# Optimization experiments

Measured on AMD Instinct MI355X. Metric: run time of the kernel, lower is better.

Reference implementation:

```python
import jax, jax.numpy as jnp
import numpy as np

DIM = 1024
NUM_HEADS = 16
HEAD_DIM = DIM // NUM_HEADS
SCALE = HEAD_DIM ** -0.5


def setup_inputs() -> dict:
    key = jax.random.key(0)
    k1, k2, k3, k4 = jax.random.split(key, 4)
    B, N = 2, 2048
    x = jax.random.normal(k1, (B, N, DIM), dtype=jnp.float32)
    # qkv: Linear(dim, 3*dim, bias=False); torch stores weight as [out, in]
    W_qkv = jax.random.normal(k2, (3 * DIM, DIM), dtype=jnp.float32) * (DIM ** -0.5)
    # proj: Linear(dim, dim, bias=True)
    W_proj = jax.random.normal(k3, (DIM, DIM), dtype=jnp.float32) * (DIM ** -0.5)
    b_proj = jax.random.normal(k4, (DIM,), dtype=jnp.float32) * 0.01
    return {"x": x, "W_qkv": W_qkv, "W_proj": W_proj, "b_proj": b_proj}


def reference(x, W_qkv, W_proj, b_proj):
    B, N, C = x.shape
    H, D = NUM_HEADS, HEAD_DIM
    # qkv projection: [B,N,3C] -> [3,B,H,N,D]
    qkv = jnp.einsum('bnc,oc->bno', x, W_qkv)
    qkv = qkv.reshape(B, N, 3, H, D).transpose(2, 0, 3, 1, 4)
    q, k, v = qkv[0] * SCALE, qkv[1], qkv[2]
    # full attention matrix [B,H,N,N] (faithful to manual impl)
    attn = jnp.einsum('bhqd,bhkd->bhqk', q, k)
    attn = jax.nn.softmax(attn, axis=-1)
    # dropout p=0.0 -> identity (eval semantics)
    out = jnp.einsum('bhqk,bhkd->bhqd', attn, v)  # [B,H,N,D]
    out = out.transpose(0, 2, 1, 3).reshape(B, N, C)
    out = jnp.einsum('bnc,oc->bno', out, W_proj) + b_proj
    return out
```

## Files before the change

kernel.cpp:

```cpp
#include <hip/hip_runtime.h>
#include <math.h>

#define BATCH 2
#define NTOK  2048
#define DIMC  1024
#define NH    16
#define HD    64
#define SOFT_K2 0.18033688011112042f

typedef __bf16 bf16;
typedef __attribute__((ext_vector_type(8))) __bf16 bf16x8;
typedef __attribute__((ext_vector_type(4))) __bf16 bf16x4;
typedef __attribute__((ext_vector_type(4))) float f32x4;

__device__ __forceinline__ void load_lds16(const void* g, void* l) {
    __builtin_amdgcn_global_load_lds(
        (const __attribute__((address_space(1))) void*)g,
        (__attribute__((address_space(3))) void*)l, 16, 0, 0);
}
__device__ __forceinline__ f32x4 mfma16(bf16x8 a, bf16x8 b, f32x4 c) {
    return __builtin_amdgcn_mfma_f32_16x16x32_bf16(a, b, c, 0, 0, 0);
}

__global__ __launch_bounds__(256) void cast3(
    const float* __restrict__ x,  const float* __restrict__ w1, const float* __restrict__ w2,
    bf16* __restrict__ xb, bf16* __restrict__ w1b, bf16* __restrict__ w2b)
{
    int blk = blockIdx.x;
    const float* src; bf16* dst; size_t base;
    if (blk < 4096)      { src = x;  dst = xb;  base = (size_t)blk * 1024; }
    else if (blk < 7168) { src = w1; dst = w1b; base = (size_t)(blk - 4096) * 1024; }
    else                 { src = w2; dst = w2b; base = (size_t)(blk - 7168) * 1024; }
    size_t i = base + (size_t)threadIdx.x * 4;
    float4 v = *(const float4*)(src + i);
    bf16x4 r;
    r[0] = (bf16)v.x; r[1] = (bf16)v.y; r[2] = (bf16)v.z; r[3] = (bf16)v.w;
    *(bf16x4*)(dst + i) = r;
}


__global__ __launch_bounds__(256, 3) void gemm_qkv(
    const bf16* __restrict__ A, const bf16* __restrict__ B,
    bf16* __restrict__ Cq, bf16* __restrict__ vt,
    int M, int N, int K)
{
    __shared__ __align__(16) bf16 smem[17408];

    const int tid  = threadIdx.x;
    const int w    = tid >> 6, lane = tid & 63;
    const int wm   = w & 1,  wn = w >> 1;
    const int m0   = blockIdx.y * 128, n0 = blockIdx.x * 128;
    const int lm   = lane & 15, quad = lane >> 4;

    const bf16* Arow = A + (size_t)(m0 + (tid & 127)) * K + (tid >> 7) * 8;
    const bf16* Brow = B + (size_t)(n0 + (tid & 127)) * K + (tid >> 7) * 8;

    bf16x8 ar[4], br[4];
#define QKV_LOADREG(kt) do {                                    \
    for (int t = 0; t < 4; ++t) {                               \
        ar[t] = *(const bf16x8*)(Arow + (kt) + t * 16);         \
        br[t] = *(const bf16x8*)(Brow + (kt) + t * 16);         \
    } } while (0)
#define QKV_DSWRITE() do {                                      \
    for (int t = 0; t < 4; ++t) {                               \
        *(bf16x8*)(smem + (t * 256 + tid) * 8) = ar[t];         \
        *(bf16x8*)(smem + 8192 + (t * 256 + tid) * 8) = br[t];  \
    } } while (0)

    f32x4 acc[4][4];
    f32x4 z4 = {0.f, 0.f, 0.f, 0.f};
#pragma unroll
    for (int i = 0; i < 4; ++i)
#pragma unroll
        for (int j = 0; j < 4; ++j) acc[i][j] = z4;

    const int NI = K / 64;
    QKV_LOADREG(0);
    QKV_DSWRITE();
    __syncthreads();
    for (int it = 0; it < NI; ++it) {
        if (it + 1 < NI) QKV_LOADREG((it + 1) * 64);
#pragma unroll
        for (int s = 0; s < 2; ++s) {
            bf16x8 af[4], bf_[4];
#pragma unroll
            for (int mi = 0; mi < 4; ++mi)
                af[mi] = *(const bf16x8*)(smem
                    + ((s * 4 + quad) * 128 + wm * 64 + mi * 16 + lm) * 8);
#pragma unroll
            for (int ni = 0; ni < 4; ++ni)
                bf_[ni] = *(const bf16x8*)(smem + 8192
                    + ((s * 4 + quad) * 128 + wn * 64 + ni * 16 + lm) * 8);
#pragma unroll
            for (int mi = 0; mi < 4; ++mi)
#pragma unroll
                for (int ni = 0; ni < 4; ++ni)
                    acc[mi][ni] = mfma16(af[mi], bf_[ni], acc[mi][ni]);
        }
        __syncthreads();
        if (it + 1 < NI) QKV_DSWRITE();
        __syncthreads();
    }
#undef QKV_LOADREG
#undef QKV_DSWRITE

    if (n0 >= 2048) {
        bf16* T = smem;
#pragma unroll
        for (int ni = 0; ni < 4; ++ni) {
            const int dl = wn * 64 + ni * 16 + lm;
#pragma unroll
            for (int mi = 0; mi < 4; ++mi)
#pragma unroll
                for (int r = 0; r < 4; ++r)
                    T[dl * 136 + wm * 64 + mi * 16 + quad * 4 + r] = (bf16)acc[mi][ni][r];
        }
        __syncthreads();
        const int gcol0 = n0 - 2048;
        const int bb = m0 >> 11, tokbase = m0 & 2047;
#pragma unroll
        for (int rep = 0; rep < 8; ++rep) {
            const int g = rep * 256 + tid;
            const int d = g >> 4, tc = g & 15;
            bf16x8 v = *(const bf16x8*)&T[d * 136 + tc * 8];
            const int gcol = gcol0 + d, hh = gcol >> 6, dd = gcol & 63;
            *(bf16x8*)(vt + ((size_t)((bb * NH + hh) * HD + dd)) * NTOK + tokbase + tc * 8) = v;
        }
    } else {
#pragma unroll
        for (int ni = 0; ni < 4; ++ni) {
            const int col = n0 + wn * 64 + ni * 16 + lm;
#pragma unroll
            for (int mi = 0; mi < 4; ++mi)
#pragma unroll
                for (int r = 0; r < 4; ++r) {
                    const int row = m0 + wm * 64 + mi * 16 + quad * 4 + r;
                    Cq[(size_t)row * N + col] = (bf16)acc[mi][ni][r];
                }
        }
    }
}

__global__ __launch_bounds__(256, 3) void gemm_proj(
    const bf16* __restrict__ A, const bf16* __restrict__ B,
    const float* __restrict__ bias, float* __restrict__ C,
    int M, int N, int K)
{
    __shared__ __align__(16) bf16 smem[12288];

    const int tid  = threadIdx.x;
    const int w    = tid >> 6, lane = tid & 63;
    const int wm   = w & 1,  wn = w >> 1;
    const int m0   = blockIdx.y * 64, n0 = blockIdx.x * 128;
    const int lm   = lane & 15, quad = lane >> 4;

    const bf16* Arow = A + (size_t)(m0 + (tid & 63)) * K + (tid >> 6) * 8;
    const bf16* Brow = B + (size_t)(n0 + (tid & 127)) * K + (tid >> 7) * 8;

    bf16x8 ar[2], br[4];
#define PROJ_LOADREG(kt) do {                                   \
    for (int t = 0; t < 2; ++t)                                 \
        ar[t] = *(const bf16x8*)(Arow + (kt) + t * 32);         \
    for (int t = 0; t < 4; ++t)                                 \
        br[t] = *(const bf16x8*)(Brow + (kt) + t * 16);         \
    } while (0)
#define PROJ_DSWRITE() do {                                     \
    for (int t = 0; t < 2; ++t)                                 \
        *(bf16x8*)(smem + (t * 256 + tid) * 8) = ar[t];         \
    for (int t = 0; t < 4; ++t)                                 \
        *(bf16x8*)(smem + 4096 + (t * 256 + tid) * 8) = br[t];  \
    } while (0)

    f32x4 acc[2][4];
    f32x4 z4 = {0.f, 0.f, 0.f, 0.f};
#pragma unroll
    for (int i = 0; i < 2; ++i)
#pragma unroll
        for (int j = 0; j < 4; ++j) acc[i][j] = z4;

    const int NI = K / 64;
    PROJ_LOADREG(0);
    PROJ_DSWRITE();
    __syncthreads();
    for (int it = 0; it < NI; ++it) {
        if (it + 1 < NI) PROJ_LOADREG((it + 1) * 64);
#pragma unroll
        for (int s = 0; s < 2; ++s) {
            bf16x8 af[2], bf_[4];
#pragma unroll
            for (int mi = 0; mi < 2; ++mi)
                af[mi] = *(const bf16x8*)(smem
                    + ((s * 4 + quad) * 64 + wm * 32 + mi * 16 + lm) * 8);
#pragma unroll
            for (int ni = 0; ni < 4; ++ni)
                bf_[ni] = *(const bf16x8*)(smem + 4096
                    + ((s * 4 + quad) * 128 + wn * 64 + ni * 16 + lm) * 8);
#pragma unroll
            for (int mi = 0; mi < 2; ++mi)
#pragma unroll
                for (int ni = 0; ni < 4; ++ni)
                    acc[mi][ni] = mfma16(af[mi], bf_[ni], acc[mi][ni]);
        }
        __syncthreads();
        if (it + 1 < NI) PROJ_DSWRITE();
        __syncthreads();
    }
#undef PROJ_LOADREG
#undef PROJ_DSWRITE

#pragma unroll
    for (int ni = 0; ni < 4; ++ni) {
        const int col = n0 + wn * 64 + ni * 16 + lm;
        const float bi = bias[col];
#pragma unroll
        for (int mi = 0; mi < 2; ++mi)
#pragma unroll
            for (int r = 0; r < 4; ++r) {
                const int row = m0 + wm * 32 + mi * 16 + quad * 4 + r;
                C[(size_t)row * N + col] = acc[mi][ni][r] + bi;
            }
    }
}

__global__ __launch_bounds__(256, 2) void attn_mfma(
    const bf16* __restrict__ qkv,
    const bf16* __restrict__ Vt,
    bf16* __restrict__ att)
{
    __shared__ __align__(16) bf16 Ks[2][64 * 64];
    __shared__ __align__(16) bf16 Vs[2][64 * 64];
    __shared__ __align__(16) bf16 Ps[2][128 * 72];

    const int n0 = blockIdx.x * 128, h = blockIdx.y, b = blockIdx.z;
    const int tid = threadIdx.x, w = tid >> 6, lane = tid & 63;
    const int lm = lane & 15, quad = lane >> 4;

    const size_t rs = (size_t)(3 * DIMC);
    const bf16* qbase  = qkv + (size_t)b * NTOK * rs + h * HD;
    const bf16* kbase  = qbase + DIMC;
    const bf16* vtbase = Vt + ((size_t)(b * NH + h) * HD) * NTOK;

    bf16x8 aq[2][2];
#pragma unroll
    for (int g = 0; g < 2; ++g)
#pragma unroll
        for (int s2 = 0; s2 < 2; ++s2)
            aq[g][s2] = *(const bf16x8*)(qbase
                + (size_t)(n0 + w * 32 + g * 16 + lm) * rs + s2 * 32 + quad * 8);

    const int l0 = (w * 2 + 0) * 64 + lane, l1 = (w * 2 + 1) * 64 + lane;
    const bf16* kg0 = kbase + (size_t)(l0 & 63) * rs + (l0 >> 6) * 8;
    const bf16* kg1 = kbase + (size_t)(l1 & 63) * rs + (l1 >> 6) * 8;
    const bf16* vg0 = vtbase + (size_t)(l0 & 63) * NTOK + (l0 >> 6) * 8;
    const bf16* vg1 = vtbase + (size_t)(l1 & 63) * NTOK + (l1 >> 6) * 8;

#define STAGE_K(tile, dst) do { \
    load_lds16(kg0 + (size_t)(tile) * 64 * rs, (dst) + (w * 2 + 0) * 512); \
    load_lds16(kg1 + (size_t)(tile) * 64 * rs, (dst) + (w * 2 + 1) * 512); } while (0)
#define STAGE_V(tile, dst) do { \
    load_lds16(vg0 + (size_t)(tile) * 64, (dst) + (w * 2 + 0) * 512); \
    load_lds16(vg1 + (size_t)(tile) * 64, (dst) + (w * 2 + 1) * 512); } while (0)

    f32x4 O[2][4];
    f32x4 z4 = {0.f, 0.f, 0.f, 0.f};
#pragma unroll
    for (int g = 0; g < 2; ++g)
#pragma unroll
        for (int ni = 0; ni < 4; ++ni) O[g][ni] = z4;
    float lsum[2][4] = {{0.f, 0.f, 0.f, 0.f}, {0.f, 0.f, 0.f, 0.f}};

#define COMPUTE_S_PS(Ksb, Psb) do {                                           \
    f32x4 S[2][4];                                                            \
    for (int g = 0; g < 2; ++g)                                               \
        for (int ni = 0; ni < 4; ++ni) S[g][ni] = z4;                         \
    for (int s2 = 0; s2 < 2; ++s2)                                            \
        for (int ni = 0; ni < 4; ++ni) {                                      \
            bf16x8 bk = *(const bf16x8*)((Ksb)                                \
                + ((s2 * 4 + quad) * 64 + ni * 16 + lm) * 8);                 \
            S[0][ni] = mfma16(aq[0][s2], bk, S[0][ni]);                       \
            S[1][ni] = mfma16(aq[1][s2], bk, S[1][ni]);                       \
        }                                                                     \
    for (int g = 0; g < 2; ++g)                                               \
        for (int ni = 0; ni < 4; ++ni)                                        \
            for (int r = 0; r < 4; ++r) {                                     \
                const float p = __builtin_amdgcn_exp2f(S[g][ni][r] * SOFT_K2);\
                (Psb)[(w * 32 + g * 16 + quad * 4 + r) * 72 + ni * 16 + lm]   \
                    = (bf16)p;                                                \
                lsum[g][r] += p;                                              \
            }                                                                 \
} while (0)

#define COMPUTE_PV(Psb, Vsb) do {                                             \
    for (int s2 = 0; s2 < 2; ++s2) {                                          \
        bf16x8 ap0 = *(const bf16x8*)((Psb)                                   \
            + (w * 32 + lm) * 72 + s2 * 32 + quad * 8);                       \
        bf16x8 ap1 = *(const bf16x8*)((Psb)                                   \
            + (w * 32 + 16 + lm) * 72 + s2 * 32 + quad * 8);                  \
        for (int ni = 0; ni < 4; ++ni) {                                      \
            bf16x8 bv = *(const bf16x8*)((Vsb)                                \
                + ((s2 * 4 + quad) * 64 + ni * 16 + lm) * 8);                 \
            O[0][ni] = mfma16(ap0, bv, O[0][ni]);                             \
            O[1][ni] = mfma16(ap1, bv, O[1][ni]);                             \
        }                                                                     \
    }                                                                         \
} while (0)

    const int NT = NTOK / 64;

    STAGE_K(0, Ks[0]);
    STAGE_V(0, Vs[0]);
    STAGE_K(1, Ks[1]);
    __syncthreads();
    COMPUTE_S_PS(Ks[0], Ps[0]);

    for (int t = 0; t < NT; ++t) {
        __syncthreads();
        if (t + 2 < NT) STAGE_K(t + 2, Ks[t & 1]);
        if (t + 1 < NT) STAGE_V(t + 1, Vs[(t + 1) & 1]);
        if (t + 1 < NT) COMPUTE_S_PS(Ks[(t + 1) & 1], Ps[(t + 1) & 1]);
        COMPUTE_PV(Ps[t & 1], Vs[t & 1]);
    }

#undef STAGE_K
#undef STAGE_V
#undef COMPUTE_S_PS
#undef COMPUTE_PV

#pragma unroll
    for (int g = 0; g < 2; ++g)
#pragma unroll
        for (int r = 0; r < 4; ++r) {
#pragma unroll
            for (int msk = 1; msk < 16; msk <<= 1)
                lsum[g][r] += __shfl_xor(lsum[g][r], msk);
        }

#pragma unroll
    for (int g = 0; g < 2; ++g)
#pragma unroll
        for (int r = 0; r < 4; ++r) {
            const float invl = 1.0f / lsum[g][r];
            const size_t row = (size_t)(b * NTOK + n0 + w * 32 + g * 16 + quad * 4 + r);
#pragma unroll
            for (int ni = 0; ni < 4; ++ni)
                att[row * DIMC + h * HD + ni * 16 + lm] = (bf16)(O[g][ni][r] * invl);
        }
}

extern "C" void kernel_launch(void* const* d_in, const int* in_sizes, int n_in,
                              void* d_out, int out_size, void* d_ws, size_t ws_size,
                              hipStream_t stream)
{
    const float* x      = (const float*)d_in[0];
    const float* W_qkv  = (const float*)d_in[1];
    const float* W_proj = (const float*)d_in[2];
    const float* b_proj = (const float*)d_in[3];
    float* out = (float*)d_out;

    char* ws = (char*)d_ws;
    bf16* xb   = (bf16*)ws;
    bf16* w1b  = (bf16*)(ws + (8u  << 20));
    bf16* w2b  = (bf16*)(ws + (14u << 20));
    bf16* qkvb = (bf16*)(ws + (16u << 20));
    bf16* vt   = (bf16*)(ws + (40u << 20));
    bf16* attb = (bf16*)(ws + (48u << 20));

    const int M = BATCH * NTOK;

    cast3<<<8192, 256, 0, stream>>>(x, W_qkv, W_proj, xb, w1b, w2b);

    gemm_qkv<<<dim3((3 * DIMC) / 128, M / 128), 256, 0, stream>>>(
        xb, w1b, qkvb, vt, M, 3 * DIMC, DIMC);

    attn_mfma<<<dim3(NTOK / 128, NH, BATCH), 256, 0, stream>>>(qkvb, vt, attb);

    gemm_proj<<<dim3(DIMC / 128, M / 64), 256, 0, stream>>>(
        attb, w2b, b_proj, out, M, DIMC, DIMC);
}
```

Measured before the change: 221.2 us.

## Stage K/V tiles through registers instead of direct global-to-LDS loads

Replaces the global_load_lds async copies of K and V tiles with register prefetch followed by explicit LDS writes, restructuring the attention loop pipeline. Tile t+2 is loaded into registers while PV runs, then written to LDS, with an extra barrier between the PV and the next S computation. This aims for better latency hiding and simpler addressing. In exchange it costs more VGPRs, a second barrier per iteration, and serializes the S and PV phases.

```diff
diff --git a/kernel.cpp b/kernel.cpp
--- a/kernel.cpp
+++ b/kernel.cpp
@@ -13,11 +13,6 @@
 typedef __attribute__((ext_vector_type(4))) __bf16 bf16x4;
 typedef __attribute__((ext_vector_type(4))) float f32x4;
 
-__device__ __forceinline__ void load_lds16(const void* g, void* l) {
-    __builtin_amdgcn_global_load_lds(
-        (const __attribute__((address_space(1))) void*)g,
-        (__attribute__((address_space(3))) void*)l, 16, 0, 0);
-}
 __device__ __forceinline__ f32x4 mfma16(bf16x8 a, bf16x8 b, f32x4 c) {
     return __builtin_amdgcn_mfma_f32_16x16x32_bf16(a, b, c, 0, 0, 0);
 }
@@ -248,18 +243,22 @@
             aq[g][s2] = *(const bf16x8*)(qbase
                 + (size_t)(n0 + w * 32 + g * 16 + lm) * rs + s2 * 32 + quad * 8);
 
-    const int l0 = (w * 2 + 0) * 64 + lane, l1 = (w * 2 + 1) * 64 + lane;
-    const bf16* kg0 = kbase + (size_t)(l0 & 63) * rs + (l0 >> 6) * 8;
-    const bf16* kg1 = kbase + (size_t)(l1 & 63) * rs + (l1 >> 6) * 8;
-    const bf16* vg0 = vtbase + (size_t)(l0 & 63) * NTOK + (l0 >> 6) * 8;
-    const bf16* vg1 = vtbase + (size_t)(l1 & 63) * NTOK + (l1 >> 6) * 8;
-
-#define STAGE_K(tile, dst) do { \
-    load_lds16(kg0 + (size_t)(tile) * 64 * rs, (dst) + (w * 2 + 0) * 512); \
-    load_lds16(kg1 + (size_t)(tile) * 64 * rs, (dst) + (w * 2 + 1) * 512); } while (0)
-#define STAGE_V(tile, dst) do { \
-    load_lds16(vg0 + (size_t)(tile) * 64, (dst) + (w * 2 + 0) * 512); \
-    load_lds16(vg1 + (size_t)(tile) * 64, (dst) + (w * 2 + 1) * 512); } while (0)
+    const bf16* kg0 = kbase + (size_t)lane * rs + (w * 2 + 0) * 8;
+    const bf16* kg1 = kbase + (size_t)lane * rs + (w * 2 + 1) * 8;
+    const bf16* vg0 = vtbase + (size_t)lane * NTOK + (w * 2 + 0) * 8;
+    const bf16* vg1 = vtbase + (size_t)lane * NTOK + (w * 2 + 1) * 8;
+
+    bf16x8 kr0, kr1, vr0, vr1;
+#define KV_LOADREG(tile) do {                                       \
+    kr0 = *(const bf16x8*)(kg0 + (size_t)(tile) * 64 * rs);         \
+    kr1 = *(const bf16x8*)(kg1 + (size_t)(tile) * 64 * rs);         \
+    vr0 = *(const bf16x8*)(vg0 + (size_t)(tile) * 64);              \
+    vr1 = *(const bf16x8*)(vg1 + (size_t)(tile) * 64); } while (0)
+#define KV_DSWRITE(buf) do {                                        \
+    *(bf16x8*)(Ks[buf] + ((w * 2 + 0) * 64 + lane) * 8) = kr0;      \
+    *(bf16x8*)(Ks[buf] + ((w * 2 + 1) * 64 + lane) * 8) = kr1;      \
+    *(bf16x8*)(Vs[buf] + ((w * 2 + 0) * 64 + lane) * 8) = vr0;      \
+    *(bf16x8*)(Vs[buf] + ((w * 2 + 1) * 64 + lane) * 8) = vr1; } while (0)
 
     f32x4 O[2][4];
     f32x4 z4 = {0.f, 0.f, 0.f, 0.f};
@@ -307,22 +306,24 @@
 
     const int NT = NTOK / 64;
 
-    STAGE_K(0, Ks[0]);
-    STAGE_V(0, Vs[0]);
-    STAGE_K(1, Ks[1]);
+    KV_LOADREG(0);
+    KV_DSWRITE(0);
     __syncthreads();
+    KV_LOADREG(1);
     COMPUTE_S_PS(Ks[0], Ps[0]);
 
     for (int t = 0; t < NT; ++t) {
-        __syncthreads();
-        if (t + 2 < NT) STAGE_K(t + 2, Ks[t & 1]);
-        if (t + 1 < NT) STAGE_V(t + 1, Vs[(t + 1) & 1]);
-        if (t + 1 < NT) COMPUTE_S_PS(Ks[(t + 1) & 1], Ps[(t + 1) & 1]);
-        COMPUTE_PV(Ps[t & 1], Vs[t & 1]);
-    }
-
-#undef STAGE_K
-#undef STAGE_V
+        const int buf = t & 1;
+        __syncthreads();
+        if (t + 1 < NT) KV_DSWRITE(buf ^ 1);
+        if (t + 2 < NT) KV_LOADREG(t + 2);
+        COMPUTE_PV(Ps[buf], Vs[buf]);
+        __syncthreads();
+        if (t + 1 < NT) COMPUTE_S_PS(Ks[buf ^ 1], Ps[buf ^ 1]);
+    }
+
+#undef KV_LOADREG
+#undef KV_DSWRITE
 #undef COMPUTE_S_PS
 #undef COMPUTE_PV
 
```

Result: no change. 224.0 us (+1.3%).
